# Kernel tuning notes

Measured on AMD Instinct MI355X. Metric: run time of the kernel, lower is better.

The kernel has to match this reference:

```python
import jax, jax.numpy as jnp
import numpy as np
from jax import lax

STRIDE = 2
PADDING = 2
EPS = 1e-5


def _conv1d(x, w):
    # x: (N, C_in, T), w: (C_out, C_in, K) -> (N, C_out, T_out)
    return lax.conv_general_dilated(
        x, w, window_strides=(STRIDE,), padding=[(PADDING, PADDING)],
        dimension_numbers=("NCH", "OIH", "NCH"))


def setup_inputs() -> dict:
    key = jax.random.key(0)
    ks = jax.random.split(key, 5)
    Batch, num_sensors, in_c, out_c, k, T, r = 32, 8, 64, 128, 5, 2048, 8
    x = jax.random.normal(ks[0], (Batch * num_sensors, in_c, T), dtype=jnp.float32)
    A_flat = jax.random.normal(ks[1], (Batch, r * in_c * k), dtype=jnp.float32) * 0.02
    B_flat = jax.random.normal(ks[2], (Batch, out_c * r), dtype=jnp.float32) * 0.02
    fan_in = in_c * k
    conv_w = jax.random.normal(ks[3], (out_c, in_c, k), dtype=jnp.float32) / np.sqrt(fan_in)
    conv_b = jax.random.normal(ks[4], (out_c,), dtype=jnp.float32) * 0.01
    gamma = jnp.ones((out_c,), dtype=jnp.float32)
    beta = jnp.zeros((out_c,), dtype=jnp.float32)
    return {"x": x, "A_flat": A_flat, "B_flat": B_flat,
            "conv_w": conv_w, "conv_b": conv_b, "gamma": gamma, "beta": beta,
            "num_sensors": num_sensors, "r": r, "lora_scale": 0.5}


def reference(x, A_flat, B_flat, conv_w, conv_b, gamma, beta, num_sensors, r, lora_scale):
    Batch = A_flat.shape[0]
    out_c, in_c, k = conv_w.shape
    T = x.shape[-1]

    # base conv1d
    out_base = _conv1d(x, conv_w) + conv_b[None, :, None]  # (B*S, out_c, T_out)

    # dynamic per-sample LoRA delta weight: delta_W = B @ A, (Batch, out_c, in_c, k)
    A = A_flat.reshape(Batch, r, in_c * k)
    B_mat = B_flat.reshape(Batch, out_c, r)
    delta_W = jnp.einsum("bor,brm->bom", B_mat, A).reshape(Batch, out_c, in_c, k)
    delta_W = delta_W * lora_scale

    # per-sample conv: sensors of one sample share that sample's delta weight
    x_b = x.reshape(Batch, num_sensors, in_c, T)
    lora_out = jax.vmap(_conv1d)(x_b, delta_W)  # (Batch, S, out_c, T_out)
    lora_out = lora_out.reshape(Batch * num_sensors, out_c, -1)

    out = jax.nn.relu(out_base + lora_out)

    # GroupNorm, num_groups = min(4, out_c) reduced until divisible
    G = min(4, out_c)
    while out_c % G != 0:
        G -= 1
    N, C, To = out.shape
    og = out.reshape(N, G, C // G, To)
    mean = og.mean(axis=(2, 3), keepdims=True)
    var = og.var(axis=(2, 3), keepdims=True)
    normed = ((og - mean) * lax.rsqrt(var + EPS)).reshape(N, C, To)
    return normed * gamma[None, :, None] + beta[None, :, None]
```

## Files before the change

### kernel.cpp

```cpp
#include <hip/hip_runtime.h>

#define T_IN 2048
#define T_OUT 1024
#define NCOL 2052
#define PITCH 36
#define EPSV 1e-5f

typedef short bf16x8 __attribute__((ext_vector_type(8)));
typedef short bf16x4 __attribute__((ext_vector_type(4)));
typedef float f32x4  __attribute__((ext_vector_type(4)));

__device__ __forceinline__ short f2bf(float f){
  unsigned u = __float_as_uint(f);
  u += 0x7fff + ((u >> 16) & 1);
  return (short)(u >> 16);
}

__global__ void build_weights(const float* __restrict__ A_flat,
                              const float* __restrict__ B_flat,
                              const float* __restrict__ conv_w,
                              const float* __restrict__ scale_p,
                              short* __restrict__ Wb){
  int idx = blockIdx.x * 256 + threadIdx.x;
  int ci = idx & 63;
  int co = (idx >> 6) & 127;
  int bj = idx >> 13;
  int b  = bj / 5;
  int j  = bj - 5 * b;
  int m  = ci * 5 + j;
  const float* Bp = B_flat + (b * 128 + co) * 8;
  const float* Ap = A_flat + b * 8 * 320 + m;
  float d = 0.f;
#pragma unroll
  for (int r = 0; r < 8; ++r) d = fmaf(Bp[r], Ap[r * 320], d);
  float w = conv_w[co * 320 + m] + scale_p[0] * d;
  Wb[idx] = f2bf(w);
}

__global__ __launch_bounds__(512, 2)
void conv_gn_mfma(const float* __restrict__ x,
                  const short* __restrict__ Wb,
                  const float* __restrict__ conv_b,
                  const float* __restrict__ gamma,
                  const float* __restrict__ beta,
                  float* __restrict__ out){
  __shared__ short xl[NCOL * PITCH];
  __shared__ float redS[8], redQ[8], bc2[2];

  const int bid    = blockIdx.x;
  const int sample = ((bid & 7) << 5) + (bid >> 5);
  const int g      = (bid >> 3) & 3;
  const int b      = sample >> 3;
  const int tid    = threadIdx.x;
  const int lane   = tid & 63;
  const int wid    = tid >> 6;
  const int l16    = lane & 15;
  const int lk     = lane >> 4;
  const int t0w    = wid << 7;

  f32x4 acc[2][8];
#pragma unroll
  for (int m2 = 0; m2 < 2; ++m2)
#pragma unroll
    for (int n = 0; n < 8; ++n) acc[m2][n] = (f32x4){0.f, 0.f, 0.f, 0.f};

  const size_t wb_base = (size_t)b * 5 * 128 * 64;

  for (int ch = 0; ch < 2; ++ch) {
    if (ch) __syncthreads();
    {
      const float* xs = x + ((size_t)sample * 64 + ch * 32 + wid * 4) * T_IN;
      if (tid < 72) {
        int cc = tid / 18, dw = tid % 18;
        int col = (cc < 2) ? cc : (2048 + cc);
        *(int*)((char*)xl + col * 72 + dw * 4) = 0;
      }
#pragma unroll 2
      for (int pass = 0; pass < 8; ++pass) {
        int cb = pass * 256 + lane * 4;
        const float4 v0 = *(const float4*)(xs + 0 * T_IN + cb);
        const float4 v1 = *(const float4*)(xs + 1 * T_IN + cb);
        const float4 v2 = *(const float4*)(xs + 2 * T_IN + cb);
        const float4 v3 = *(const float4*)(xs + 3 * T_IN + cb);
        bf16x4 p0 = {f2bf(v0.x), f2bf(v1.x), f2bf(v2.x), f2bf(v3.x)};
        bf16x4 p1 = {f2bf(v0.y), f2bf(v1.y), f2bf(v2.y), f2bf(v3.y)};
        bf16x4 p2 = {f2bf(v0.z), f2bf(v1.z), f2bf(v2.z), f2bf(v3.z)};
        bf16x4 p3 = {f2bf(v0.w), f2bf(v1.w), f2bf(v2.w), f2bf(v3.w)};
        short* dst = &xl[(cb + 2) * PITCH + wid * 4];
        *(bf16x4*)(dst)             = p0;
        *(bf16x4*)(dst + PITCH)     = p1;
        *(bf16x4*)(dst + 2 * PITCH) = p2;
        *(bf16x4*)(dst + 3 * PITCH) = p3;
      }
    }
    __syncthreads();
#pragma unroll
    for (int j = 0; j < 5; ++j) {
      const short* apb = Wb + wb_base + ((size_t)j * 128 + g * 32) * 64 + ch * 32 + lk * 8;
      bf16x8 a0 = *(const bf16x8*)(apb + (size_t)(l16)      * 64);
      bf16x8 a1 = *(const bf16x8*)(apb + (size_t)(l16 + 16) * 64);
#pragma unroll
      for (int n = 0; n < 8; ++n) {
        int c = 2 * (t0w + n * 16 + l16) + j;
        const short* bp = &xl[c * PITCH + lk * 8];
        bf16x4 lo = *(const bf16x4*)bp;
        bf16x4 hi = *(const bf16x4*)(bp + 4);
        bf16x8 bfr = {lo[0], lo[1], lo[2], lo[3], hi[0], hi[1], hi[2], hi[3]};
        acc[0][n] = __builtin_amdgcn_mfma_f32_16x16x32_bf16(a0, bfr, acc[0][n], 0, 0, 0);
        acc[1][n] = __builtin_amdgcn_mfma_f32_16x16x32_bf16(a1, bfr, acc[1][n], 0, 0, 0);
      }
    }
  }

  float cb_[2][4], ga_[2][4], be_[2][4];
#pragma unroll
  for (int m2 = 0; m2 < 2; ++m2)
#pragma unroll
    for (int r = 0; r < 4; ++r) {
      int co = g * 32 + m2 * 16 + lk * 4 + r;
      cb_[m2][r] = conv_b[co];
      ga_[m2][r] = gamma[co];
      be_[m2][r] = beta[co];
    }
  float s1 = 0.f, s2 = 0.f;
#pragma unroll
  for (int m2 = 0; m2 < 2; ++m2)
#pragma unroll
    for (int n = 0; n < 8; ++n)
#pragma unroll
      for (int r = 0; r < 4; ++r) {
        float v = acc[m2][n][r] + cb_[m2][r];
        v = v > 0.f ? v : 0.f;
        acc[m2][n][r] = v;
        s1 += v;
        s2 = fmaf(v, v, s2);
      }
#pragma unroll
  for (int off = 32; off; off >>= 1) {
    s1 += __shfl_down(s1, off);
    s2 += __shfl_down(s2, off);
  }
  if (lane == 0) { redS[wid] = s1; redQ[wid] = s2; }
  __syncthreads();
  if (tid == 0) {
    float a = 0.f, q = 0.f;
#pragma unroll
    for (int w = 0; w < 8; ++w) { a += redS[w]; q += redQ[w]; }
    float mean = a * (1.f / 32768.f);
    float var  = q * (1.f / 32768.f) - mean * mean;
    bc2[0] = mean;
    bc2[1] = rsqrtf(var + EPSV);
  }
  __syncthreads();
  const float mean = bc2[0], inv = bc2[1];
  float* ob = out + (size_t)sample * 128 * 1024;
#pragma unroll
  for (int m2 = 0; m2 < 2; ++m2)
#pragma unroll
    for (int r = 0; r < 4; ++r) {
      int co = g * 32 + m2 * 16 + lk * 4 + r;
      float aa = ga_[m2][r] * inv;
      float bb = be_[m2][r] - mean * aa;
      float* orow = ob + (size_t)co * 1024 + t0w + l16;
#pragma unroll
      for (int n = 0; n < 8; ++n)
        orow[n * 16] = acc[m2][n][r] * aa + bb;
    }
}

extern "C" void kernel_launch(void* const* d_in, const int* in_sizes, int n_in,
                              void* d_out, int out_size, void* d_ws, size_t ws_size,
                              hipStream_t stream) {
  const float* x       = (const float*)d_in[0];
  const float* A_flat  = (const float*)d_in[1];
  const float* B_flat  = (const float*)d_in[2];
  const float* conv_w  = (const float*)d_in[3];
  const float* conv_b  = (const float*)d_in[4];
  const float* gamma   = (const float*)d_in[5];
  const float* beta    = (const float*)d_in[6];
  const float* scale_p = (const float*)d_in[9];

  float* out = (float*)d_out;
  short* Wb  = (short*)d_ws;

  build_weights<<<5120, 256, 0, stream>>>(A_flat, B_flat, conv_w, scale_p, Wb);
  conv_gn_mfma<<<1024, 512, 0, stream>>>(x, Wb, conv_b, gamma, beta, out);
}
```

Baseline: 90.84 us.

## Split input staging into even/odd LDS halves over time to cut LDS footprint

The input tile is now staged in four phases (two time halves by two channel halves), with even and odd time columns de-interleaved into separate LDS arrays. This shrinks shared memory per block from about 148KB to about 74KB so launch bounds can request 4 blocks per SM. It also switches packing to paired bf16 conversions and changes the block-to-sample mapping. In exchange there are more barriers and extra halo loads per phase, and less L2 reuse of a sample's input across its group blocks.

```diff
diff --git a/kernel.cpp b/kernel.cpp
--- a/kernel.cpp
+++ b/kernel.cpp
@@ -1,10 +1,9 @@
 #include <hip/hip_runtime.h>
-
-#define T_IN 2048
-#define T_OUT 1024
-#define NCOL 2052
+#include <hip/hip_bf16.h>
+
+#define EPSV 1e-5f
 #define PITCH 36
-#define EPSV 1e-5f
+#define PCOLS 516
 
 typedef short bf16x8 __attribute__((ext_vector_type(8)));
 typedef short bf16x4 __attribute__((ext_vector_type(4)));
@@ -14,6 +13,10 @@
   unsigned u = __float_as_uint(f);
   u += 0x7fff + ((u >> 16) & 1);
   return (short)(u >> 16);
+}
+__device__ __forceinline__ int pk2(float a, float b){
+  __hip_bfloat162 h = __float22bfloat162_rn(float2{a, b});
+  return *reinterpret_cast<int*>(&h);
 }
 
 __global__ void build_weights(const float* __restrict__ A_flat,
@@ -37,75 +40,83 @@
   Wb[idx] = f2bf(w);
 }
 
-__global__ __launch_bounds__(512, 2)
+__global__ __launch_bounds__(512, 4)
 void conv_gn_mfma(const float* __restrict__ x,
                   const short* __restrict__ Wb,
                   const float* __restrict__ conv_b,
                   const float* __restrict__ gamma,
                   const float* __restrict__ beta,
                   float* __restrict__ out){
-  __shared__ short xl[NCOL * PITCH];
+  __shared__ short xe[PCOLS * PITCH];
+  __shared__ short xo[PCOLS * PITCH];
   __shared__ float redS[8], redQ[8], bc2[2];
 
   const int bid    = blockIdx.x;
-  const int sample = ((bid & 7) << 5) + (bid >> 5);
-  const int g      = (bid >> 3) & 3;
+  const int sample = bid & 255;
+  const int g      = bid >> 8;
   const int b      = sample >> 3;
   const int tid    = threadIdx.x;
   const int lane   = tid & 63;
   const int wid    = tid >> 6;
   const int l16    = lane & 15;
   const int lk     = lane >> 4;
-  const int t0w    = wid << 7;
 
   f32x4 acc[2][8];
 #pragma unroll
   for (int m2 = 0; m2 < 2; ++m2)
 #pragma unroll
-    for (int n = 0; n < 8; ++n) acc[m2][n] = (f32x4){0.f, 0.f, 0.f, 0.f};
+    for (int n = 0; n < 8; ++n) acc[m2][n] = (f32x4){0.f,0.f,0.f,0.f};
 
   const size_t wb_base = (size_t)b * 5 * 128 * 64;
-
-  for (int ch = 0; ch < 2; ++ch) {
-    if (ch) __syncthreads();
+  const float* xsamp = x + (size_t)sample * 64 * 2048;
+
+#pragma unroll
+  for (int ph = 0; ph < 4; ++ph) {
+    const int th = ph >> 1;
+    const int ch = ph & 1;
+
+    if (ph) __syncthreads();
     {
-      const float* xs = x + ((size_t)sample * 64 + ch * 32 + wid * 4) * T_IN;
-      if (tid < 72) {
-        int cc = tid / 18, dw = tid % 18;
-        int col = (cc < 2) ? cc : (2048 + cc);
-        *(int*)((char*)xl + col * 72 + dw * 4) = 0;
-      }
+      const float* xbase = xsamp + (size_t)(ch * 32) * 2048;
+      const float* xr = xbase + (size_t)(wid * 4) * 2048 + th * 1024;
 #pragma unroll 2
       for (int pass = 0; pass < 8; ++pass) {
-        int cb = pass * 256 + lane * 4;
-        const float4 v0 = *(const float4*)(xs + 0 * T_IN + cb);
-        const float4 v1 = *(const float4*)(xs + 1 * T_IN + cb);
-        const float4 v2 = *(const float4*)(xs + 2 * T_IN + cb);
-        const float4 v3 = *(const float4*)(xs + 3 * T_IN + cb);
-        bf16x4 p0 = {f2bf(v0.x), f2bf(v1.x), f2bf(v2.x), f2bf(v3.x)};
-        bf16x4 p1 = {f2bf(v0.y), f2bf(v1.y), f2bf(v2.y), f2bf(v3.y)};
-        bf16x4 p2 = {f2bf(v0.z), f2bf(v1.z), f2bf(v2.z), f2bf(v3.z)};
-        bf16x4 p3 = {f2bf(v0.w), f2bf(v1.w), f2bf(v2.w), f2bf(v3.w)};
-        short* dst = &xl[(cb + 2) * PITCH + wid * 4];
-        *(bf16x4*)(dst)             = p0;
-        *(bf16x4*)(dst + PITCH)     = p1;
-        *(bf16x4*)(dst + 2 * PITCH) = p2;
-        *(bf16x4*)(dst + 3 * PITCH) = p3;
+        int c0 = pass * 128 + lane * 2;
+        float2 v0 = *(const float2*)(xr + 0 * 2048 + c0);
+        float2 v1 = *(const float2*)(xr + 1 * 2048 + c0);
+        float2 v2 = *(const float2*)(xr + 2 * 2048 + c0);
+        float2 v3 = *(const float2*)(xr + 3 * 2048 + c0);
+        int pcol = pass * 64 + lane + 1;
+        int2 ev = { pk2(v0.x, v1.x), pk2(v2.x, v3.x) };
+        int2 od = { pk2(v0.y, v1.y), pk2(v2.y, v3.y) };
+        *(int2*)(xe + pcol * PITCH + wid * 4) = ev;
+        *(int2*)(xo + pcol * PITCH + wid * 4) = od;
+      }
+      if (tid < 128) {
+        int which = tid >> 5;
+        int ci    = tid & 31;
+        int xc    = th * 1024 + ((which < 2) ? (which - 2) : (1024 + (which & 1)));
+        float v = (xc >= 0 && xc < 2048) ? xbase[(size_t)ci * 2048 + xc] : 0.f;
+        short* arr = (which & 1) ? xo : xe;
+        arr[((which < 2) ? 0 : 513) * PITCH + ci] = f2bf(v);
       }
     }
     __syncthreads();
 #pragma unroll
     for (int j = 0; j < 5; ++j) {
-      const short* apb = Wb + wb_base + ((size_t)j * 128 + g * 32) * 64 + ch * 32 + lk * 8;
-      bf16x8 a0 = *(const bf16x8*)(apb + (size_t)(l16)      * 64);
+      const short* apb = Wb + wb_base + (size_t)(j * 128 + g * 32) * 64 + ch * 32 + lk * 8;
+      bf16x8 a0 = *(const bf16x8*)(apb + (size_t)l16 * 64);
       bf16x8 a1 = *(const bf16x8*)(apb + (size_t)(l16 + 16) * 64);
-#pragma unroll
-      for (int n = 0; n < 8; ++n) {
-        int c = 2 * (t0w + n * 16 + l16) + j;
-        const short* bp = &xl[c * PITCH + lk * 8];
+      const short* arr = (j & 1) ? xo : xe;
+      const int joff = (j & 1) ? ((j - 1) >> 1) : (j >> 1);
+#pragma unroll
+      for (int nn = 0; nn < 4; ++nn) {
+        int tloc = wid * 64 + nn * 16 + l16;
+        const short* bp = arr + (tloc + joff) * PITCH + lk * 8;
         bf16x4 lo = *(const bf16x4*)bp;
         bf16x4 hi = *(const bf16x4*)(bp + 4);
-        bf16x8 bfr = {lo[0], lo[1], lo[2], lo[3], hi[0], hi[1], hi[2], hi[3]};
+        bf16x8 bfr = {lo[0],lo[1],lo[2],lo[3],hi[0],hi[1],hi[2],hi[3]};
+        const int n = th * 4 + nn;
         acc[0][n] = __builtin_amdgcn_mfma_f32_16x16x32_bf16(a0, bfr, acc[0][n], 0, 0, 0);
         acc[1][n] = __builtin_amdgcn_mfma_f32_16x16x32_bf16(a1, bfr, acc[1][n], 0, 0, 0);
       }
@@ -161,10 +172,12 @@
       int co = g * 32 + m2 * 16 + lk * 4 + r;
       float aa = ga_[m2][r] * inv;
       float bb = be_[m2][r] - mean * aa;
-      float* orow = ob + (size_t)co * 1024 + t0w + l16;
-#pragma unroll
-      for (int n = 0; n < 8; ++n)
-        orow[n * 16] = acc[m2][n][r] * aa + bb;
+      float* orow = ob + (size_t)co * 1024 + l16;
+#pragma unroll
+      for (int n = 0; n < 8; ++n) {
+        int t = (n >> 2) * 512 + wid * 64 + (n & 3) * 16;
+        orow[t] = acc[m2][n][r] * aa + bb;
+      }
     }
 }
 
```

Result: slower. 129.5 us (+42.6%).
